# Kernel optimization log

Hardware: AMD Instinct MI355X
Metric: run time of the kernel (lower is better)

Reference implementation:

```python
import jax, jax.numpy as jnp
import numpy as np

ORDER = 3  # truncation level; num_components = ORDER*(ORDER+1)//2 = 6 (independent weights)


def setup_inputs() -> dict:
    key = jax.random.key(0)
    k1, k2, k3 = jax.random.split(key, 3)
    B, T, D, F = 64, 4096, 128, 64
    C = ORDER * (ORDER + 1) // 2
    sequences = jax.random.normal(k1, (B, T, D), dtype=jnp.float32)
    # ls2t_uniform-style init: scaled uniform per component
    kernel = jax.random.normal(k2, (C, D, F), dtype=jnp.float32) / np.sqrt(D)
    bias = jax.random.normal(k3, (C, F), dtype=jnp.float32) * 0.01
    return {"sequences": sequences, "kernel": kernel, "bias": bias}


def _exclusive_cumsum(x, axis):
    # exclusive cumsum = inclusive cumsum minus self (avoids concat/pad allocs)
    return jnp.cumsum(x, axis=axis) - x


def reference(sequences, kernel, bias):
    # sequences: [B, T, D]; kernel: [C, D, F]; bias: [C, F]
    # M[c] = sequences @ kernel[c] + bias[c]  -> [C, B, T, F]
    M = jnp.einsum('btd,cdf->cbtf', sequences, kernel) + bias[:, None, None, :]
    # Level 1: plain sum over time of first component
    Y = [jnp.sum(M[0], axis=1)]  # [B, F]
    k = 1
    for m in range(1, ORDER):
        R = M[k]
        k += 1
        for _ in range(m):
            # iterated-sum recursion: strictly-lower-triangular (exclusive) cumsum over time
            R = M[k] * _exclusive_cumsum(R, axis=1)
            k += 1
        Y.append(jnp.sum(R, axis=1))
    return jnp.stack(Y, axis=-1)  # [B, F, ORDER]
```

## Files before the change

kernel.cpp:

```cpp
#include <hip/hip_runtime.h>
#include <hip/hip_bf16.h>


#define B_ 64
#define T_ 4096
#define D_ 128
#define F_ 64
#define TB 512
#define TGROUPS (T_ / TB)
#define CHT 16
#define NITER (TB / CHT)
#define TPB 256
#define RING 4

typedef __attribute__((ext_vector_type(8))) short short8v;
typedef __attribute__((ext_vector_type(4))) float f32x4;

__device__ __forceinline__ unsigned short bfb(float x) {
    __hip_bfloat16 h = __float2bfloat16(x);
    unsigned short u;
    __builtin_memcpy(&u, &h, 2);
    return u;
}

#define BAR() asm volatile("s_waitcnt lgkmcnt(0)\n\ts_barrier" ::: "memory")

__global__ __launch_bounds__(TPB)
void ls2t_kernel(const float* __restrict__ seq,
                 const float* __restrict__ kern,
                 const float* __restrict__ bias,
                 float* __restrict__ ws)
{
    __shared__ unsigned short slds[RING][CHT * D_];

    const int tid  = threadIdx.x;
    const int tg   = blockIdx.x >> 1;
    const int cg   = blockIdx.x & 1;
    const int b    = blockIdx.y;
    const int lane = tid & 63;
    const int wv   = tid >> 6;
    const int fr   = lane & 15;
    const int lg   = lane >> 4;
    const int f    = wv * 16 + fr;

    short8v bfrag[3][4];
    float bc[3];
    #pragma unroll
    for (int cc = 0; cc < 3; ++cc) {
        const int c = cg * 3 + cc;
        bc[cc] = bias[c * F_ + f];
        #pragma unroll
        for (int ks = 0; ks < 4; ++ks) {
            const float* kp = kern + ((size_t)c * D_ + ks * 32 + lg * 8) * F_ + f;
            short8v bf;
            #pragma unroll
            for (int j = 0; j < 8; ++j) bf[j] = (short)bfb(kp[(size_t)j * F_]);
            bfrag[cc][ks] = bf;
        }
    }

    const float* sbase = seq + ((size_t)b * T_ + (size_t)tg * TB) * D_;

    const float* gp[2];
    int woff[2];
    #pragma unroll
    for (int k = 0; k < 2; ++k) {
        const int u  = k * TPB + tid;
        const int sr = u >> 5, c4 = u & 31;
        gp[k]   = sbase + ((size_t)((sr >> 2) * 128 + (sr & 3))) * D_ + c4 * 4;
        woff[k] = sr * D_ + 8 * ((c4 >> 1) ^ (sr & 7)) + 4 * (c4 & 1);
    }

    struct VSet { float4 a, b; };
    VSet vA, vB;
    auto issue = [&](int i, VSet& vs) {
        vs.a = *reinterpret_cast<const float4*>(gp[0] + (size_t)i * 4 * D_);
        vs.b = *reinterpret_cast<const float4*>(gp[1] + (size_t)i * 4 * D_);
    };
    auto wst = [&](int bufi, const VSet& vs) {
        unsigned short* L = &slds[bufi][0];
        uint2 pa, pb;
        pa.x = __builtin_amdgcn_perm(__float_as_uint(vs.a.y),
                                     __float_as_uint(vs.a.x), 0x07060302u);
        pa.y = __builtin_amdgcn_perm(__float_as_uint(vs.a.w),
                                     __float_as_uint(vs.a.z), 0x07060302u);
        pb.x = __builtin_amdgcn_perm(__float_as_uint(vs.b.y),
                                     __float_as_uint(vs.b.x), 0x07060302u);
        pb.y = __builtin_amdgcn_perm(__float_as_uint(vs.b.w),
                                     __float_as_uint(vs.b.z), 0x07060302u);
        *reinterpret_cast<uint2*>(&L[woff[0]]) = pa;
        *reinterpret_cast<uint2*>(&L[woff[1]]) = pb;
    };

    float x0 = 0.f, x1 = 0.f, x2 = 0.f, x3 = 0.f, x4 = 0.f, x5 = 0.f;

    auto compute = [&](int bufi) {
        f32x4 acc[3];
        #pragma unroll
        for (int cc = 0; cc < 3; ++cc)
            acc[cc] = (f32x4){bc[cc], bc[cc], bc[cc], bc[cc]};

        #pragma unroll
        for (int ks = 0; ks < 4; ++ks) {
            short8v a = *reinterpret_cast<const short8v*>(
                &slds[bufi][fr * D_ + 8 * ((ks * 4 + lg) ^ (fr & 7))]);
            #pragma unroll
            for (int cc = 0; cc < 3; ++cc)
                acc[cc] = __builtin_amdgcn_mfma_f32_16x16x32_bf16(
                    a, bfrag[cc][ks], acc[cc], 0, 0, 0);
        }

        #pragma unroll
        for (int r = 0; r < 4; ++r) {
            float p = acc[0][r], q = acc[1][r], rr = acc[2][r];
            x5 = fmaf(rr, x3, x5);
            x4 = fmaf(rr, x1, x4);
            x3 = fmaf(q,  x0, x3);
            x2 += rr;
            x1 += q;
            x0 += p;
        }
    };

    issue(0, vA);
    issue(1, vB);
    wst(0, vA);
    issue(2, vA);
    BAR();

    #pragma unroll 1
    for (int g = 0; g < 28; g += 4) {
        wst(1, vB); issue(g + 3, vB); BAR(); compute(0);
        wst(2, vA); issue(g + 4, vA); BAR(); compute(1);
        wst(3, vB); issue(g + 5, vB); BAR(); compute(2);
        wst(0, vA); issue(g + 6, vA); BAR(); compute(3);
    }
    wst(1, vB); issue(31, vB); BAR(); compute(0);
    wst(2, vA);                BAR(); compute(1);
    wst(3, vB);                BAR(); compute(2);
    compute(3);

    #pragma unroll
    for (int m = 16; m <= 32; m <<= 1) {
        float o0 = __shfl_xor(x0, m), o1 = __shfl_xor(x1, m);
        float o2 = __shfl_xor(x2, m), o3 = __shfl_xor(x3, m);
        float o4 = __shfl_xor(x4, m), o5 = __shfl_xor(x5, m);
        const bool up = (lane & m) != 0;
        float A0 = up ? o0 : x0, B0 = up ? x0 : o0;
        float A1 = up ? o1 : x1, B1 = up ? x1 : o1;
        float A2 = up ? o2 : x2, B2 = up ? x2 : o2;
        float A3 = up ? o3 : x3, B3 = up ? x3 : o3;
        float A4 = up ? o4 : x4, B4 = up ? x4 : o4;
        float A5 = up ? o5 : x5, B5 = up ? x5 : o5;
        x5 = A5 + B5 + A3 * B2 + A0 * B4;
        x4 = A4 + B4 + A1 * B2;
        x3 = A3 + B3 + A0 * B1;
        x2 = A2 + B2;
        x1 = A1 + B1;
        x0 = A0 + B0;
    }

    if (lg == 0) {
        float* wp = ws + (((size_t)b * TGROUPS + tg) * F_ + f) * 10;
        if (cg == 0) {
            wp[0] = x0; wp[1] = x1; wp[2] = x2; wp[3] = x4;
        } else {
            wp[4] = x0; wp[5] = x1; wp[6] = x2;
            wp[7] = x3; wp[8] = x4; wp[9] = x5;
        }
    }
}

struct St { float a0, s1, s2, q2, su, sv, sw, qvu, qwv, qwvu; };

__device__ __forceinline__ St mergeSt(const St& A, const St& B) {
    St r;
    r.a0   = A.a0 + B.a0;
    r.q2   = A.q2 + B.q2 + A.s1 * B.s2;
    r.s1   = A.s1 + B.s1;
    r.s2   = A.s2 + B.s2;
    r.qwvu = A.qwvu + B.qwvu + A.qvu * B.sw + A.su * B.qwv;
    r.qwv  = A.qwv + B.qwv + A.sv * B.sw;
    r.qvu  = A.qvu + B.qvu + A.su * B.sv;
    r.su   = A.su + B.su;
    r.sv   = A.sv + B.sv;
    r.sw   = A.sw + B.sw;
    return r;
}

__global__ __launch_bounds__(64)
void ls2t_fold_kernel(const float* __restrict__ ws, float* __restrict__ out)
{
    const int b = blockIdx.x;
    const int f = threadIdx.x;
    St A = {0, 0, 0, 0, 0, 0, 0, 0, 0, 0};
    #pragma unroll
    for (int g = 0; g < TGROUPS; ++g) {
        const float* rp = ws + (((size_t)b * TGROUPS + g) * F_ + f) * 10;
        St r = {rp[0], rp[1], rp[2], rp[3], rp[4],
                rp[5], rp[6], rp[7], rp[8], rp[9]};
        A = mergeSt(A, r);
    }
    float* op = out + ((size_t)b * F_ + f) * 3;
    op[0] = A.a0;
    op[1] = A.q2;
    op[2] = A.qwvu;
}

extern "C" void kernel_launch(void* const* d_in, const int* in_sizes, int n_in,
                              void* d_out, int out_size, void* d_ws, size_t ws_size,
                              hipStream_t stream) {
    const float* seq  = (const float*)d_in[0];
    const float* kern = (const float*)d_in[1];
    const float* bias = (const float*)d_in[2];
    float* out = (float*)d_out;
    float* ws  = (float*)d_ws;

    dim3 g1(TGROUPS * 2, B_);
    ls2t_kernel<<<g1, TPB, 0, stream>>>(seq, kern, bias, ws);
    ls2t_fold_kernel<<<B_, F_, 0, stream>>>(ws, out);
}
```

Before: 49.95 us.

## Use direct global-to-LDS loads and merge component groups into one block

```diff
diff --git a/kernel.cpp b/kernel.cpp
--- a/kernel.cpp
+++ b/kernel.cpp
@@ -10,7 +10,7 @@
 #define TGROUPS (T_ / TB)
 #define CHT 16
 #define NITER (TB / CHT)
-#define TPB 256
+#define TPB 512
 #define RING 4
 
 typedef __attribute__((ext_vector_type(8))) short short8v;
@@ -24,6 +24,7 @@
 }
 
 #define BAR() asm volatile("s_waitcnt lgkmcnt(0)\n\ts_barrier" ::: "memory")
+#define VW(n) asm volatile("s_waitcnt vmcnt(" #n ")" ::: "memory")
 
 __global__ __launch_bounds__(TPB)
 void ls2t_kernel(const float* __restrict__ seq,
@@ -31,14 +32,15 @@
                  const float* __restrict__ bias,
                  float* __restrict__ ws)
 {
-    __shared__ unsigned short slds[RING][CHT * D_];
+    __shared__ float slds[RING][CHT * D_];
 
     const int tid  = threadIdx.x;
-    const int tg   = blockIdx.x >> 1;
-    const int cg   = blockIdx.x & 1;
+    const int tg   = blockIdx.x;
     const int b    = blockIdx.y;
     const int lane = tid & 63;
-    const int wv   = tid >> 6;
+    const int w    = tid >> 6;
+    const int cg   = w >> 2;
+    const int wv   = w & 3;
     const int fr   = lane & 15;
     const int lg   = lane >> 4;
     const int f    = wv * 16 + fr;
@@ -61,40 +63,24 @@
 
     const float* sbase = seq + ((size_t)b * T_ + (size_t)tg * TB) * D_;
 
-    const float* gp[2];
-    int woff[2];
-    #pragma unroll
-    for (int k = 0; k < 2; ++k) {
-        const int u  = k * TPB + tid;
-        const int sr = u >> 5, c4 = u & 31;
-        gp[k]   = sbase + ((size_t)((sr >> 2) * 128 + (sr & 3))) * D_ + c4 * 4;
-        woff[k] = sr * D_ + 8 * ((c4 >> 1) ^ (sr & 7)) + 4 * (c4 & 1);
-    }
-
-    struct VSet { float4 a, b; };
-    VSet vA, vB;
-    auto issue = [&](int i, VSet& vs) {
-        vs.a = *reinterpret_cast<const float4*>(gp[0] + (size_t)i * 4 * D_);
-        vs.b = *reinterpret_cast<const float4*>(gp[1] + (size_t)i * 4 * D_);
+    const int r_lane = 2 * w + (lane >> 5);
+    const int u_lane = lane & 31;
+    const int gu     = (u_lane & 24) | ((u_lane ^ r_lane) & 7);
+    const float* gsrc0 = sbase
+        + ((size_t)((r_lane >> 2) * 128 + (r_lane & 3))) * D_ + gu * 4;
+
+    auto issue = [&](int i, int bufi) {
+        const float* src = gsrc0 + (size_t)i * 4 * D_;
+        void* dst = (void*)&slds[bufi][w * 256];
+        __builtin_amdgcn_global_load_lds(
+            (const __attribute__((address_space(1))) void*)src,
+            (__attribute__((address_space(3))) void*)dst, 16, 0, 0);
     };
-    auto wst = [&](int bufi, const VSet& vs) {
-        unsigned short* L = &slds[bufi][0];
-        uint2 pa, pb;
-        pa.x = __builtin_amdgcn_perm(__float_as_uint(vs.a.y),
-                                     __float_as_uint(vs.a.x), 0x07060302u);
-        pa.y = __builtin_amdgcn_perm(__float_as_uint(vs.a.w),
-                                     __float_as_uint(vs.a.z), 0x07060302u);
-        pb.x = __builtin_amdgcn_perm(__float_as_uint(vs.b.y),
-                                     __float_as_uint(vs.b.x), 0x07060302u);
-        pb.y = __builtin_amdgcn_perm(__float_as_uint(vs.b.w),
-                                     __float_as_uint(vs.b.z), 0x07060302u);
-        *reinterpret_cast<uint2*>(&L[woff[0]]) = pa;
-        *reinterpret_cast<uint2*>(&L[woff[1]]) = pb;
-    };
 
     float x0 = 0.f, x1 = 0.f, x2 = 0.f, x3 = 0.f, x4 = 0.f, x5 = 0.f;
 
     auto compute = [&](int bufi) {
+        const float* L = &slds[bufi][0];
         f32x4 acc[3];
         #pragma unroll
         for (int cc = 0; cc < 3; ++cc)
@@ -102,8 +88,21 @@
 
         #pragma unroll
         for (int ks = 0; ks < 4; ++ks) {
-            short8v a = *reinterpret_cast<const short8v*>(
-                &slds[bufi][fr * D_ + 8 * ((ks * 4 + lg) ^ (fr & 7))]);
+            const int u0 = ks * 8 + lg * 2;
+            const int s0 = (u0 & 24) | ((u0 ^ fr) & 7);
+            const int s1 = ((u0 + 1) & 24) | (((u0 + 1) ^ fr) & 7);
+            float4 fa = *reinterpret_cast<const float4*>(&L[fr * 128 + s0 * 4]);
+            float4 fb = *reinterpret_cast<const float4*>(&L[fr * 128 + s1 * 4]);
+            uint4 pk;
+            pk.x = __builtin_amdgcn_perm(__float_as_uint(fa.y),
+                                         __float_as_uint(fa.x), 0x07060302u);
+            pk.y = __builtin_amdgcn_perm(__float_as_uint(fa.w),
+                                         __float_as_uint(fa.z), 0x07060302u);
+            pk.z = __builtin_amdgcn_perm(__float_as_uint(fb.y),
+                                         __float_as_uint(fb.x), 0x07060302u);
+            pk.w = __builtin_amdgcn_perm(__float_as_uint(fb.w),
+                                         __float_as_uint(fb.z), 0x07060302u);
+            short8v a = *reinterpret_cast<short8v*>(&pk);
             #pragma unroll
             for (int cc = 0; cc < 3; ++cc)
                 acc[cc] = __builtin_amdgcn_mfma_f32_16x16x32_bf16(
@@ -122,23 +121,18 @@
         }
     };
 
-    issue(0, vA);
-    issue(1, vB);
-    wst(0, vA);
-    issue(2, vA);
-    BAR();
+    issue(0, 0); issue(1, 1); issue(2, 2);
 
     #pragma unroll 1
-    for (int g = 0; g < 28; g += 4) {
-        wst(1, vB); issue(g + 3, vB); BAR(); compute(0);
-        wst(2, vA); issue(g + 4, vA); BAR(); compute(1);
-        wst(3, vB); issue(g + 5, vB); BAR(); compute(2);
-        wst(0, vA); issue(g + 6, vA); BAR(); compute(3);
-    }
-    wst(1, vB); issue(31, vB); BAR(); compute(0);
-    wst(2, vA);                BAR(); compute(1);
-    wst(3, vB);                BAR(); compute(2);
-    compute(3);
+    for (int i = 0; i < NITER - 3; ++i) {
+        VW(2);
+        BAR();
+        issue(i + 3, (i + 3) & 3);
+        compute(i & 3);
+    }
+    VW(2); BAR(); compute(1);
+    VW(1); BAR(); compute(2);
+    VW(0); BAR(); compute(3);
 
     #pragma unroll
     for (int m = 16; m <= 32; m <<= 1) {
@@ -216,7 +210,7 @@
     float* out = (float*)d_out;
     float* ws  = (float*)d_ws;
 
-    dim3 g1(TGROUPS * 2, B_);
+    dim3 g1(TGROUPS, B_);
     ls2t_kernel<<<g1, TPB, 0, stream>>>(seq, kern, bias, ws);
     ls2t_fold_kernel<<<B_, F_, 0, stream>>>(ws, out);
 }
```

Result: faster. 43.43 us (-13.0%).
